# Optimization experiments

Measured on AMD Instinct MI355X. Metric: run time of the kernel, lower is better.

Reference implementation:

```python
import jax, jax.numpy as jnp
import numpy as np
import math

T, B = 1024, 512
DIM_S, DIM_C, DIM_Y = 32, 32, 16
DIM_Z, DIM_H, RANK = 256, 256, 8
ALPHA_Z, ALPHA_H = 0.01, 0.1


def setup_inputs() -> dict:
    key = jax.random.key(0)
    ks = jax.random.split(key, 9)
    return {
        "s": jax.random.normal(ks[0], (T, B, DIM_S), jnp.float32),
        "c": jax.random.normal(ks[1], (T, B, DIM_C), jnp.float32),
        "W_zz": jax.random.normal(ks[2], (DIM_Z, DIM_Z), jnp.float32) * math.sqrt(1.0 / DIM_Z),
        "Wz_in": jax.random.normal(ks[3], (DIM_Z, DIM_S + DIM_C), jnp.float32) * math.sqrt(2.0 / (DIM_Z + DIM_S + DIM_C)),
        "bz_in": jnp.zeros((DIM_Z,), jnp.float32),
        "Wz_out": jax.random.normal(ks[4], (RANK, DIM_Z), jnp.float32) * math.sqrt(2.0 / (RANK + DIM_Z)),
        "bz_out": jnp.zeros((RANK,), jnp.float32),
        "U": jax.random.normal(ks[5], (DIM_H, RANK), jnp.float32) * ((1.0 / DIM_H) ** 0.25 / math.sqrt(RANK)),
        "V": jax.random.normal(ks[6], (DIM_H, RANK), jnp.float32) * ((1.0 / DIM_H) ** 0.25 / math.sqrt(RANK)),
        "W_in": jax.random.normal(ks[7], (DIM_H, DIM_S), jnp.float32) * math.sqrt(2.0 / (DIM_H + DIM_S)),
        "b_in": jnp.zeros((DIM_H,), jnp.float32),
        "W_out": jax.random.normal(ks[8], (DIM_Y, DIM_H), jnp.float32) * math.sqrt(2.0 / (DIM_H + DIM_Y)),
        "b_out": jnp.zeros((DIM_Y,), jnp.float32),
    }


def reference(s, c, W_zz, Wz_in, bz_in, Wz_out, bz_out, U, V, W_in, b_in, W_out, b_out):
    # sig_r = 0 -> noise terms vanish (module default).
    def step(carry, sc_t):
        z, h = carry
        s_t, c_t = sc_t
        tmp = jnp.tanh(z) @ W_zz.T + jnp.concatenate([s_t, c_t], axis=-1) @ Wz_in.T + bz_in
        z = (1.0 - ALPHA_Z) * z + ALPHA_Z * tmp  # [B, Z]
        signal = jax.nn.sigmoid(z @ Wz_out.T + bz_out)  # [B, R]
        # einsum('br,hr,kr,bk->bh') == ((tanh(h) @ V) * signal) @ U.T
        tmp = ((jnp.tanh(h) @ V) * signal) @ U.T + s_t @ W_in.T + b_in
        h = (1.0 - ALPHA_H) * h + ALPHA_H * tmp  # [B, H]
        out = jnp.tanh(h) @ W_out.T + b_out  # [B, Y]
        return (z, h), (out, z, h)

    z0 = jnp.zeros((s.shape[1], DIM_Z), s.dtype)
    h0 = jnp.zeros((s.shape[1], DIM_H), s.dtype)
    _, (outputs, states_z, states_h) = jax.lax.scan(step, (z0, h0), (s, c))
    states = jnp.concatenate([states_z, states_h], axis=-1)  # [T, B, Z+H]
    return outputs, states
```

## Files before the change

kernel.cpp:

```cpp
#include <hip/hip_runtime.h>
#include <math.h>

#define T_STEPS 1024
#define BATCH   512
#define DZ      256
#define DH      256
#define RANK    8
#define DY      16


typedef _Float16 f16;
typedef _Float16 h2 __attribute__((ext_vector_type(2)));

__device__ __forceinline__ h2 pack2(float a, float b) {
    h2 r; r.x = (f16)a; r.y = (f16)b; return r;
}
__device__ __forceinline__ h2 bc(unsigned u) { return __builtin_bit_cast(h2, u); }

__device__ __forceinline__ float dot2(h2 a, h2 b, float c) {
#if __has_builtin(__builtin_amdgcn_fdot2)
    return __builtin_amdgcn_fdot2(a, b, c, false);
#else
    return fmaf((float)a.x, (float)b.x, fmaf((float)a.y, (float)b.y, c));
#endif
}

__device__ __forceinline__ float fast_tanh(float x) {
    const float e = __expf(2.0f * x);
    return 1.0f - 2.0f / (e + 1.0f);
}

__global__ __launch_bounds__(512, 1)
void nmrnn_main(
    const float* __restrict__ s, const float* __restrict__ c,
    const float* __restrict__ W_zz, const float* __restrict__ Wz_in,
    const float* __restrict__ bz_in, const float* __restrict__ Wz_out,
    const float* __restrict__ bz_out, const float* __restrict__ U,
    const float* __restrict__ V, const float* __restrict__ W_in,
    const float* __restrict__ b_in,
    float* __restrict__ states)
{
    __shared__ __align__(16) f16 tzh[2][2][DZ];
    __shared__ __align__(16) f16 thh[2][2][DH];
    __shared__ __align__(16) f16 sclh[2][2][64];
    __shared__ __align__(16) f16 vt16[RANK][DH];
    __shared__ __align__(16) f16 pz16[RANK][DZ];
    __shared__ __align__(16) f16 pzi16[RANK][64];
    __shared__ float gl[2][RANK];

    const int tid = threadIdx.x;
    const int i   = tid & 255;
    const int bb  = tid >> 8;
    const int l32 = tid & 31;
    const int b0  = blockIdx.x * 2;
    const int gg = tid >> 5;
    const int rr = gg & 7;
    const int rb = gg >> 3;

    h2 wzz[128];
    #pragma unroll
    for (int m = 0; m < 64; ++m) {
        const float4 v4 = *(const float4*)&W_zz[i * 256 + (m << 2)];
        wzz[2 * m]     = pack2(v4.x, v4.y);
        wzz[2 * m + 1] = pack2(v4.z, v4.w);
    }
    h2 wzi[32];
    #pragma unroll
    for (int m = 0; m < 16; ++m) {
        const float4 v4 = *(const float4*)&Wz_in[i * 64 + (m << 2)];
        wzi[2 * m]     = pack2(v4.x, v4.y);
        wzi[2 * m + 1] = pack2(v4.z, v4.w);
    }
    h2 wi[16];
    #pragma unroll
    for (int m = 0; m < 8; ++m) {
        const float4 v4 = *(const float4*)&W_in[i * 32 + (m << 2)];
        wi[2 * m]     = pack2(v4.x, v4.y);
        wi[2 * m + 1] = pack2(v4.z, v4.w);
    }
    float uu[8];
    {
        const float4 a = *(const float4*)&U[i * 8];
        const float4 b4 = *(const float4*)&U[i * 8 + 4];
        uu[0]=a.x; uu[1]=a.y; uu[2]=a.z; uu[3]=a.w;
        uu[4]=b4.x; uu[5]=b4.y; uu[6]=b4.z; uu[7]=b4.w;
    }

    if (tid < 256) {
        #pragma unroll
        for (int r = 0; r < RANK; ++r) vt16[r][tid] = (f16)V[tid * RANK + r];
    }
    #pragma unroll
    for (int p = 0; p < 4; ++p) {
        const int e = p * 512 + tid;
        const int r = e >> 8, col = e & 255;
        const float* wrow = &Wz_out[r * 256];
        float a0 = 0.f, a1 = 0.f;
        #pragma unroll 4
        for (int k = 0; k < 256; k += 2) {
            a0 = fmaf(wrow[k],     W_zz[k * 256 + col],       a0);
            a1 = fmaf(wrow[k + 1], W_zz[(k + 1) * 256 + col], a1);
        }
        pz16[r][col] = (f16)(a0 + a1);
    }
    {
        const int r = tid >> 6, j = tid & 63;
        const float* wrow = &Wz_out[r * 256];
        float a0 = 0.f, a1 = 0.f;
        #pragma unroll 4
        for (int k = 0; k < 256; k += 2) {
            a0 = fmaf(wrow[k],     Wz_in[k * 64 + j],       a0);
            a1 = fmaf(wrow[k + 1], Wz_in[(k + 1) * 64 + j], a1);
        }
        pzi16[r][j] = (f16)(a0 + a1);
    }
    tzh[0][bb][i] = (f16)0.f;
    thh[0][bb][i] = (f16)0.f;
    if (tid < 128) {
        const int b2 = tid >> 6, rI = tid & 63;
        const size_t base = (size_t)(b0 + b2) * 32;
        sclh[0][b2][rI] = (f16)((rI < 32) ? s[base + rI] : c[base + rI - 32]);
    }

    const float bz = bz_in[i];
    const float bh = b_in[i];
    float z_r = 0.f, h_r = 0.f;

    float czb, rzb;
    {
        float cz = 0.f;
        #pragma unroll
        for (int m = 0; m < 8; ++m) {
            const int k = l32 + 32 * m;
            cz = fmaf(bz_in[k], Wz_out[rr * 256 + k], cz);
        }
        #pragma unroll
        for (int off = 16; off >= 1; off >>= 1) cz += __shfl_xor(cz, off);
        const float bzo_r = bz_out[rr];
        czb = cz + bzo_r;
        rzb = bzo_r;
    }

    int cur = 0;
    __syncthreads();

    for (int t = 0; t < T_STEPS; ++t) {
        float pfn = 0.f;
        if (tid < 128 && t + 1 < T_STEPS) {
            const int b2 = tid >> 6, rI = tid & 63;
            const size_t base = ((size_t)(t + 1) * BATCH + b0 + b2) * 32;
            pfn = (rI < 32) ? s[base + rI] : c[base + rI - 32];
        }

        {
            const h2* tp  = (const h2*)&thh[cur][rb][0];
            const h2* vp  = (const h2*)&vt16[rr][0];
            const h2* tzp = (const h2*)&tzh[cur][rb][0];
            const h2* pzp = (const h2*)&pz16[rr][0];
            float hp0 = 0.f, hp1 = 0.f, zp0 = 0.f, zp1 = 0.f;
            hp0 = dot2(tp[l32],       vp[l32],       hp0);
            hp1 = dot2(tp[l32 + 32],  vp[l32 + 32],  hp1);
            hp0 = dot2(tp[l32 + 64],  vp[l32 + 64],  hp0);
            hp1 = dot2(tp[l32 + 96],  vp[l32 + 96],  hp1);
            zp0 = dot2(tzp[l32],      pzp[l32],      zp0);
            zp1 = dot2(tzp[l32 + 32], pzp[l32 + 32], zp1);
            zp0 = dot2(tzp[l32 + 64], pzp[l32 + 64], zp0);
            zp1 = dot2(tzp[l32 + 96], pzp[l32 + 96], zp1);
            const h2* scp  = (const h2*)&sclh[cur][rb][0];
            const h2* pzip = (const h2*)&pzi16[rr][0];
            zp0 = dot2(scp[l32], pzip[l32], zp0);
            float hp = hp0 + hp1, zp = zp0 + zp1;
            #pragma unroll
            for (int off = 16; off >= 1; off >>= 1) {
                hp += __shfl_xor(hp, off);
                zp += __shfl_xor(zp, off);
            }
            rzb = 0.99f * rzb + 0.01f * (zp + czb);
            const float sg = 1.0f / (1.0f + __expf(-rzb));
            if (l32 == 0) gl[rb][rr] = sg * hp;
        }

        float az0 = 0.f, az1 = 0.f, az2 = 0.f, az3 = 0.f;
        float wh0 = 0.f, wh1 = 0.f;
        {
            const uint4* tz = (const uint4*)&tzh[cur][bb][0];
            #pragma unroll
            for (int m = 0; m < 32; ++m) {
                const uint4 u = tz[m];
                az0 = dot2(wzz[4 * m + 0], bc(u.x), az0);
                az1 = dot2(wzz[4 * m + 1], bc(u.y), az1);
                az2 = dot2(wzz[4 * m + 2], bc(u.z), az2);
                az3 = dot2(wzz[4 * m + 3], bc(u.w), az3);
            }
            const uint4* sp = (const uint4*)&sclh[cur][bb][0];
            #pragma unroll
            for (int m = 0; m < 8; ++m) {
                const uint4 u = sp[m];
                az0 = dot2(wzi[4 * m + 0], bc(u.x), az0);
                az1 = dot2(wzi[4 * m + 1], bc(u.y), az1);
                az2 = dot2(wzi[4 * m + 2], bc(u.z), az2);
                az3 = dot2(wzi[4 * m + 3], bc(u.w), az3);
            }
            #pragma unroll
            for (int m = 0; m < 4; ++m) {
                const uint4 u = sp[m];
                wh0 = dot2(wi[4 * m + 0], bc(u.x), wh0);
                wh1 = dot2(wi[4 * m + 1], bc(u.y), wh1);
                wh0 = dot2(wi[4 * m + 2], bc(u.z), wh0);
                wh1 = dot2(wi[4 * m + 3], bc(u.w), wh1);
            }
        }
        __syncthreads();

        const float zsum = (az0 + az1) + (az2 + az3) + bz;
        z_r = 0.99f * z_r + 0.01f * zsum;
        tzh[cur ^ 1][bb][i] = (f16)fast_tanh(z_r);
        states[((size_t)t * BATCH + b0 + bb) * 512 + i] = z_r;

        const float4 g0 = *(const float4*)&gl[bb][0];
        const float4 g1 = *(const float4*)&gl[bb][4];
        float hs0 = wh0 + bh, hs1 = wh1;
        hs0 = fmaf(uu[0], g0.x, hs0); hs1 = fmaf(uu[1], g0.y, hs1);
        hs0 = fmaf(uu[2], g0.z, hs0); hs1 = fmaf(uu[3], g0.w, hs1);
        hs0 = fmaf(uu[4], g1.x, hs0); hs1 = fmaf(uu[5], g1.y, hs1);
        hs0 = fmaf(uu[6], g1.z, hs0); hs1 = fmaf(uu[7], g1.w, hs1);
        h_r = 0.9f * h_r + 0.1f * (hs0 + hs1);
        thh[cur ^ 1][bb][i] = (f16)fast_tanh(h_r);
        states[((size_t)t * BATCH + b0 + bb) * 512 + 256 + i] = h_r;

        if (tid < 128 && t + 1 < T_STEPS)
            sclh[cur ^ 1][tid >> 6][tid & 63] = (f16)pfn;
        cur ^= 1;
        __syncthreads();
    }
}

__global__ __launch_bounds__(256)
void nmrnn_out(const float* __restrict__ states,
               const float* __restrict__ W_out,
               const float* __restrict__ b_out,
               float* __restrict__ out)
{
    __shared__ __align__(16) f16 th[16][264];
    __shared__ __align__(16) f16 wo[16][258];
    __shared__ float bo[DY];

    const int tid = threadIdx.x;
    #pragma unroll
    for (int it = 0; it < 16; ++it) {
        const int e = it * 256 + tid;
        wo[e >> 8][e & 255] = (f16)W_out[e];
    }
    if (tid < DY) bo[tid] = b_out[tid];

    const size_t row0 = (size_t)blockIdx.x * 16;
    #pragma unroll
    for (int it = 0; it < 16; ++it) {
        const float v = states[(row0 + it) * 512 + 256 + tid];
        th[it][tid] = (f16)fast_tanh(v);
    }
    __syncthreads();

    const int r = tid >> 4, y = tid & 15;
    const h2* tp = (const h2*)&th[r][0];
    const h2* wp = (const h2*)&wo[y][0];
    float a0 = 0.f, a1 = 0.f, a2 = 0.f, a3 = 0.f;
    #pragma unroll
    for (int p = 0; p < 128; p += 4) {
        a0 = dot2(tp[p],     wp[p],     a0);
        a1 = dot2(tp[p + 1], wp[p + 1], a1);
        a2 = dot2(tp[p + 2], wp[p + 2], a2);
        a3 = dot2(tp[p + 3], wp[p + 3], a3);
    }
    out[row0 * 16 + tid] = (a0 + a1) + (a2 + a3) + bo[y];
}

extern "C" void kernel_launch(void* const* d_in, const int* in_sizes, int n_in,
                              void* d_out, int out_size, void* d_ws, size_t ws_size,
                              hipStream_t stream) {
    const float* s     = (const float*)d_in[0];
    const float* c     = (const float*)d_in[1];
    const float* W_zz  = (const float*)d_in[2];
    const float* Wz_in = (const float*)d_in[3];
    const float* bz_in = (const float*)d_in[4];
    const float* Wz_out= (const float*)d_in[5];
    const float* bz_out= (const float*)d_in[6];
    const float* U     = (const float*)d_in[7];
    const float* V     = (const float*)d_in[8];
    const float* W_in  = (const float*)d_in[9];
    const float* b_in  = (const float*)d_in[10];
    const float* W_out = (const float*)d_in[11];
    const float* b_out = (const float*)d_in[12];

    float* out    = (float*)d_out;
    float* states = out + (size_t)T_STEPS * BATCH * DY;

    hipLaunchKernelGGL(nmrnn_main, dim3(BATCH / 2), dim3(512), 0, stream,
                       s, c, W_zz, Wz_in, bz_in, Wz_out, bz_out, U, V,
                       W_in, b_in, states);

    hipLaunchKernelGGL(nmrnn_out, dim3(T_STEPS * BATCH / 16), dim3(256), 0,
                       stream, states, W_out, b_out, out);
}
```

Baseline: 2.154 ms.

## Split each output row's K-range across thread pairs to halve weight registers

Thread mapping changes from one thread per (batch, row) to a pair of adjacent threads per row. Each thread holds half of the W_zz/Wz_in/W_in K-range and computes partial sums for both batch rows, combined with a lane-xor shuffle. This halves per-thread weight register footprint (128 to 64 h2 for W_zz), which can reduce spills or raise occupancy. The cost is extra LDS reads of both batch rows' activations and added shuffles on the serial per-step critical path.

```diff
diff --git a/kernel.cpp b/kernel.cpp
--- a/kernel.cpp
+++ b/kernel.cpp
@@ -49,38 +49,38 @@
     __shared__ float gl[2][RANK];
 
     const int tid = threadIdx.x;
-    const int i   = tid & 255;
-    const int bb  = tid >> 8;
+    const int p   = tid & 1;
+    const int i   = tid >> 1;
     const int l32 = tid & 31;
     const int b0  = blockIdx.x * 2;
     const int gg = tid >> 5;
     const int rr = gg & 7;
     const int rb = gg >> 3;
 
-    h2 wzz[128];
-    #pragma unroll
-    for (int m = 0; m < 64; ++m) {
-        const float4 v4 = *(const float4*)&W_zz[i * 256 + (m << 2)];
+    h2 wzz[64];
+    #pragma unroll
+    for (int m = 0; m < 32; ++m) {
+        const float4 v4 = *(const float4*)&W_zz[i * 256 + (p << 7) + (m << 2)];
         wzz[2 * m]     = pack2(v4.x, v4.y);
         wzz[2 * m + 1] = pack2(v4.z, v4.w);
     }
-    h2 wzi[32];
-    #pragma unroll
-    for (int m = 0; m < 16; ++m) {
-        const float4 v4 = *(const float4*)&Wz_in[i * 64 + (m << 2)];
+    h2 wzi[16];
+    #pragma unroll
+    for (int m = 0; m < 8; ++m) {
+        const float4 v4 = *(const float4*)&Wz_in[i * 64 + (p << 5) + (m << 2)];
         wzi[2 * m]     = pack2(v4.x, v4.y);
         wzi[2 * m + 1] = pack2(v4.z, v4.w);
     }
-    h2 wi[16];
-    #pragma unroll
-    for (int m = 0; m < 8; ++m) {
-        const float4 v4 = *(const float4*)&W_in[i * 32 + (m << 2)];
+    h2 wi[8];
+    #pragma unroll
+    for (int m = 0; m < 4; ++m) {
+        const float4 v4 = *(const float4*)&W_in[i * 32 + (p << 4) + (m << 2)];
         wi[2 * m]     = pack2(v4.x, v4.y);
         wi[2 * m + 1] = pack2(v4.z, v4.w);
     }
     float uu[8];
     {
-        const float4 a = *(const float4*)&U[i * 8];
+        const float4 a  = *(const float4*)&U[i * 8];
         const float4 b4 = *(const float4*)&U[i * 8 + 4];
         uu[0]=a.x; uu[1]=a.y; uu[2]=a.z; uu[3]=a.w;
         uu[4]=b4.x; uu[5]=b4.y; uu[6]=b4.z; uu[7]=b4.w;
@@ -91,8 +91,8 @@
         for (int r = 0; r < RANK; ++r) vt16[r][tid] = (f16)V[tid * RANK + r];
     }
     #pragma unroll
-    for (int p = 0; p < 4; ++p) {
-        const int e = p * 512 + tid;
+    for (int pp = 0; pp < 4; ++pp) {
+        const int e = pp * 512 + tid;
         const int r = e >> 8, col = e & 255;
         const float* wrow = &Wz_out[r * 256];
         float a0 = 0.f, a1 = 0.f;
@@ -114,8 +114,8 @@
         }
         pzi16[r][j] = (f16)(a0 + a1);
     }
-    tzh[0][bb][i] = (f16)0.f;
-    thh[0][bb][i] = (f16)0.f;
+    tzh[0][p][i] = (f16)0.f;
+    thh[0][p][i] = (f16)0.f;
     if (tid < 128) {
         const int b2 = tid >> 6, rI = tid & 63;
         const size_t base = (size_t)(b0 + b2) * 32;
@@ -180,53 +180,78 @@
             if (l32 == 0) gl[rb][rr] = sg * hp;
         }
 
-        float az0 = 0.f, az1 = 0.f, az2 = 0.f, az3 = 0.f;
+        float a00 = 0.f, a01 = 0.f, a10 = 0.f, a11 = 0.f;
         float wh0 = 0.f, wh1 = 0.f;
         {
-            const uint4* tz = (const uint4*)&tzh[cur][bb][0];
+            const uint4* tz0 = (const uint4*)&tzh[cur][0][p << 7];
+            const uint4* tz1 = (const uint4*)&tzh[cur][1][p << 7];
             #pragma unroll
-            for (int m = 0; m < 32; ++m) {
-                const uint4 u = tz[m];
-                az0 = dot2(wzz[4 * m + 0], bc(u.x), az0);
-                az1 = dot2(wzz[4 * m + 1], bc(u.y), az1);
-                az2 = dot2(wzz[4 * m + 2], bc(u.z), az2);
-                az3 = dot2(wzz[4 * m + 3], bc(u.w), az3);
+            for (int m = 0; m < 16; ++m) {
+                const uint4 u0 = tz0[m];
+                const uint4 u1 = tz1[m];
+                a00 = dot2(wzz[4 * m + 0], bc(u0.x), a00);
+                a01 = dot2(wzz[4 * m + 1], bc(u0.y), a01);
+                a00 = dot2(wzz[4 * m + 2], bc(u0.z), a00);
+                a01 = dot2(wzz[4 * m + 3], bc(u0.w), a01);
+                a10 = dot2(wzz[4 * m + 0], bc(u1.x), a10);
+                a11 = dot2(wzz[4 * m + 1], bc(u1.y), a11);
+                a10 = dot2(wzz[4 * m + 2], bc(u1.z), a10);
+                a11 = dot2(wzz[4 * m + 3], bc(u1.w), a11);
             }
-            const uint4* sp = (const uint4*)&sclh[cur][bb][0];
-            #pragma unroll
-            for (int m = 0; m < 8; ++m) {
-                const uint4 u = sp[m];
-                az0 = dot2(wzi[4 * m + 0], bc(u.x), az0);
-                az1 = dot2(wzi[4 * m + 1], bc(u.y), az1);
-                az2 = dot2(wzi[4 * m + 2], bc(u.z), az2);
-                az3 = dot2(wzi[4 * m + 3], bc(u.w), az3);
-            }
+            const uint4* sp0 = (const uint4*)&sclh[cur][0][p << 5];
+            const uint4* sp1 = (const uint4*)&sclh[cur][1][p << 5];
             #pragma unroll
             for (int m = 0; m < 4; ++m) {
-                const uint4 u = sp[m];
-                wh0 = dot2(wi[4 * m + 0], bc(u.x), wh0);
-                wh1 = dot2(wi[4 * m + 1], bc(u.y), wh1);
-                wh0 = dot2(wi[4 * m + 2], bc(u.z), wh0);
-                wh1 = dot2(wi[4 * m + 3], bc(u.w), wh1);
+                const uint4 u0 = sp0[m];
+                const uint4 u1 = sp1[m];
+                a00 = dot2(wzi[4 * m + 0], bc(u0.x), a00);
+                a01 = dot2(wzi[4 * m + 1], bc(u0.y), a01);
+                a00 = dot2(wzi[4 * m + 2], bc(u0.z), a00);
+                a01 = dot2(wzi[4 * m + 3], bc(u0.w), a01);
+                a10 = dot2(wzi[4 * m + 0], bc(u1.x), a10);
+                a11 = dot2(wzi[4 * m + 1], bc(u1.y), a11);
+                a10 = dot2(wzi[4 * m + 2], bc(u1.z), a10);
+                a11 = dot2(wzi[4 * m + 3], bc(u1.w), a11);
             }
-        }
+            const uint4* w0p = (const uint4*)&sclh[cur][0][p << 4];
+            const uint4* w1p = (const uint4*)&sclh[cur][1][p << 4];
+            #pragma unroll
+            for (int m = 0; m < 2; ++m) {
+                const uint4 u0 = w0p[m];
+                const uint4 u1 = w1p[m];
+                wh0 = dot2(wi[4 * m + 0], bc(u0.x), wh0);
+                wh0 = dot2(wi[4 * m + 1], bc(u0.y), wh0);
+                wh0 = dot2(wi[4 * m + 2], bc(u0.z), wh0);
+                wh0 = dot2(wi[4 * m + 3], bc(u0.w), wh0);
+                wh1 = dot2(wi[4 * m + 0], bc(u1.x), wh1);
+                wh1 = dot2(wi[4 * m + 1], bc(u1.y), wh1);
+                wh1 = dot2(wi[4 * m + 2], bc(u1.z), wh1);
+                wh1 = dot2(wi[4 * m + 3], bc(u1.w), wh1);
+            }
+        }
+        float z0 = a00 + a01;
+        float z1 = a10 + a11;
+        z0  += __shfl_xor(z0, 1);
+        z1  += __shfl_xor(z1, 1);
+        wh0 += __shfl_xor(wh0, 1);
+        wh1 += __shfl_xor(wh1, 1);
         __syncthreads();
 
-        const float zsum = (az0 + az1) + (az2 + az3) + bz;
+        const float zsum = (p == 0 ? z0 : z1) + bz;
         z_r = 0.99f * z_r + 0.01f * zsum;
-        tzh[cur ^ 1][bb][i] = (f16)fast_tanh(z_r);
-        states[((size_t)t * BATCH + b0 + bb) * 512 + i] = z_r;
-
-        const float4 g0 = *(const float4*)&gl[bb][0];
-        const float4 g1 = *(const float4*)&gl[bb][4];
-        float hs0 = wh0 + bh, hs1 = wh1;
+        tzh[cur ^ 1][p][i] = (f16)fast_tanh(z_r);
+        states[((size_t)t * BATCH + b0 + p) * 512 + i] = z_r;
+
+        const float4 g0 = *(const float4*)&gl[p][0];
+        const float4 g1 = *(const float4*)&gl[p][4];
+        float hs0 = (p == 0 ? wh0 : wh1) + bh, hs1 = 0.f;
         hs0 = fmaf(uu[0], g0.x, hs0); hs1 = fmaf(uu[1], g0.y, hs1);
         hs0 = fmaf(uu[2], g0.z, hs0); hs1 = fmaf(uu[3], g0.w, hs1);
         hs0 = fmaf(uu[4], g1.x, hs0); hs1 = fmaf(uu[5], g1.y, hs1);
         hs0 = fmaf(uu[6], g1.z, hs0); hs1 = fmaf(uu[7], g1.w, hs1);
         h_r = 0.9f * h_r + 0.1f * (hs0 + hs1);
-        thh[cur ^ 1][bb][i] = (f16)fast_tanh(h_r);
-        states[((size_t)t * BATCH + b0 + bb) * 512 + 256 + i] = h_r;
+        thh[cur ^ 1][p][i] = (f16)fast_tanh(h_r);
+        states[((size_t)t * BATCH + b0 + p) * 512 + 256 + i] = h_r;
 
         if (tid < 128 && t + 1 < T_STEPS)
             sclh[cur ^ 1][tid >> 6][tid & 63] = (f16)pfn;
@@ -266,11 +291,11 @@
     const h2* wp = (const h2*)&wo[y][0];
     float a0 = 0.f, a1 = 0.f, a2 = 0.f, a3 = 0.f;
     #pragma unroll
-    for (int p = 0; p < 128; p += 4) {
-        a0 = dot2(tp[p],     wp[p],     a0);
-        a1 = dot2(tp[p + 1], wp[p + 1], a1);
-        a2 = dot2(tp[p + 2], wp[p + 2], a2);
-        a3 = dot2(tp[p + 3], wp[p + 3], a3);
+    for (int pp = 0; pp < 128; pp += 4) {
+        a0 = dot2(tp[pp],     wp[pp],     a0);
+        a1 = dot2(tp[pp + 1], wp[pp + 1], a1);
+        a2 = dot2(tp[pp + 2], wp[pp + 2], a2);
+        a3 = dot2(tp[pp + 3], wp[pp + 3], a3);
     }
     out[row0 * 16 + tid] = (a0 + a1) + (a2 + a3) + bo[y];
 }
```

Result: slower. 2.303 ms (+6.9%).
